# Performance work log

Hardware: AMD Instinct MI355X
Metric: run time of the kernel (lower is better)

Reference implementation:

```python
import jax, jax.numpy as jnp
import numpy as np

N, E, B = 100000, 1600000, 256
IN, H, C = 7, 128, 2
BN_EPS = 1e-5


def setup_inputs() -> dict:
    key = jax.random.key(0)
    ks = jax.random.split(key, 16)
    p = lambda k, s: jax.random.normal(k, s, jnp.float32) * 0.05
    return {
        "x": jax.random.normal(ks[0], (N, IN), jnp.float32),
        "edge_index": jax.random.randint(ks[1], (2, E), 0, N, dtype=jnp.int32),
        "edge_attr": jax.random.normal(ks[2], (E,), jnp.float32),
        "batch": jnp.sort(jax.random.randint(ks[3], (N,), 0, B, dtype=jnp.int32)),
        # GINConv layer 0 MLP: Linear(IN,H) -> ReLU -> Linear(H,H)
        "W0a": p(ks[4], (IN, H)), "b0a": jnp.zeros((H,), jnp.float32),
        "W0b": p(ks[5], (H, H)), "b0b": jnp.zeros((H,), jnp.float32),
        # GINConv layers 1,2 MLPs: Linear(H,H) -> ReLU -> Linear(H,H)
        "W1a": p(ks[6], (H, H)), "b1a": jnp.zeros((H,), jnp.float32),
        "W1b": p(ks[7], (H, H)), "b1b": jnp.zeros((H,), jnp.float32),
        "W2a": p(ks[8], (H, H)), "b2a": jnp.zeros((H,), jnp.float32),
        "W2b": p(ks[9], (H, H)), "b2b": jnp.zeros((H,), jnp.float32),
        # JumpingKnowledge 'cat' projection: Linear(3H, H)
        "Wjk": p(ks[10], (3 * H, H)), "bjk": jnp.zeros((H,), jnp.float32),
        # classifier MLP([H, 2H, C], norm='batch_norm') in eval mode
        "Wc1": p(ks[11], (H, 2 * H)), "bc1": jnp.zeros((2 * H,), jnp.float32),
        "gamma": jnp.ones((2 * H,), jnp.float32),
        "beta": jnp.zeros((2 * H,), jnp.float32),
        "rmean": p(ks[12], (2 * H,)),
        "rvar": jnp.ones((2 * H,), jnp.float32),
        "Wc2": p(ks[13], (2 * H, C)), "bc2": jnp.zeros((C,), jnp.float32),
    }


def _gin_layer(x, src, dst, Wa, ba, Wb, bb):
    # GINConv, eps=0 (train_eps=False): mlp(x_i + sum_{j->i} x_j)
    agg = jax.ops.segment_sum(x[src], dst, num_segments=N)  # [N, d]
    h = x + agg
    h = jax.nn.relu(h @ Wa + ba) @ Wb + bb  # PyG MLP, plain_last, norm=None
    return jax.nn.relu(h)  # BasicGNN inter-layer activation (jk mode: all layers)


def reference(x, edge_index, edge_attr, batch,
              W0a, b0a, W0b, b0b, W1a, b1a, W1b, b1b, W2a, b2a, W2b, b2b,
              Wjk, bjk, Wc1, bc1, gamma, beta, rmean, rvar, Wc2, bc2):
    # NOTE: GINConv does not support edge_weight; PyG BasicGNN drops edge_attr.
    src, dst = edge_index[0], edge_index[1]
    x1 = _gin_layer(x, src, dst, W0a, b0a, W0b, b0b)
    x2 = _gin_layer(x1, src, dst, W1a, b1a, W1b, b1b)
    x3 = _gin_layer(x2, src, dst, W2a, b2a, W2b, b2b)
    h = jnp.concatenate([x1, x2, x3], axis=1) @ Wjk + bjk  # jk='cat' + lin
    pooled = jax.ops.segment_sum(h, batch, num_segments=B)  # global_add_pool [B, H]
    z = pooled @ Wc1 + bc1
    z = (z - rmean) * jax.lax.rsqrt(rvar + BN_EPS) * gamma + beta  # BN eval
    z = jax.nn.relu(z)  # dropout = identity in eval
    return z @ Wc2 + bc2  # [B, C]
```

## Files before the change

kernel.cpp:

```cpp
#include <hip/hip_runtime.h>

#define NN 100000
#define EE 1600000
#define BB 256
#define IN_F 7
#define HH 128
#define NBKT 391
#define BIN_CHUNK 4096
#define BCAP 8192
#define MROWS 16
#define MTHR 128
#define NSB 98

typedef unsigned int uint;
typedef unsigned short ushort;
typedef __attribute__((ext_vector_type(8))) short short8;
typedef __attribute__((ext_vector_type(4))) float f32x4;


__device__ __forceinline__ float bflo(uint u) { return __uint_as_float(u << 16); }
__device__ __forceinline__ float bfhi(uint u) { return __uint_as_float(u & 0xFFFF0000u); }
__device__ __forceinline__ ushort f2bf(float x) {
    uint u = __float_as_uint(x);
    u = (u + 0x7FFFu + ((u >> 16) & 1u)) >> 16;
    return (ushort)u;
}
__device__ __forceinline__ uint packsplit(float v) {
    ushort h = f2bf(v);
    float hf = __uint_as_float((uint)h << 16);
    ushort lo = f2bf(v - hf);
    return ((uint)h << 16) | (uint)lo;
}


__global__ __launch_bounds__(256) void prep(
        const float* __restrict__ w0, const float* __restrict__ w1,
        const float* __restrict__ w2, const float* __restrict__ w3,
        const float* __restrict__ w4, const float* __restrict__ w5,
        const float* __restrict__ w6, const float* __restrict__ w7,
        ushort* __restrict__ hiB, ushort* __restrict__ loB,
        int* __restrict__ deg, int* __restrict__ bcnt,
        float* __restrict__ pooled, int* __restrict__ agg, int n) {
    int b = blockIdx.x, t = threadIdx.x;
    if (b < 512) {
        const float* ws[8] = {w0, w1, w2, w3, w4, w5, w6, w7};
        int gidx = b * 256 + t;
        int mi = gidx >> 14;
        int idx = gidx & 16383;
        int j = idx & 7, l = (idx >> 3) & 63, blk = idx >> 9;
        int kc = blk >> 3, nt = blk & 7;
        int k = kc * 32 + (l >> 4) * 8 + j;
        int nn = nt * 16 + (l & 15);
        float f = ws[mi][k * 128 + nn];
        ushort h = f2bf(f);
        float hf = __uint_as_float((uint)h << 16);
        hiB[gidx] = h;
        loB[gidx] = f2bf(f - hf);
    } else if (b < 512 + NSB) {
        int i = (b - 512) * 1024 + t * 4;
        if (i + 3 < n) {
            *(int4*)&deg[i] = make_int4(0, 0, 0, 0);
        } else {
            #pragma unroll
            for (int k = 0; k < 4; ++k) if (i + k < n) deg[i + k] = 0;
        }
    } else if (b < 512 + NSB + 32) {
        int i = (b - 512 - NSB) * 1024 + t * 4;
        *(float4*)&pooled[i] = make_float4(0.f, 0.f, 0.f, 0.f);
    } else {
        for (int i = t; i < NBKT; i += 256) bcnt[i] = 0;
        if (t < NSB) agg[t] = 0;
    }
}


__global__ __launch_bounds__(256) void bin_count(const int* __restrict__ ei,
        int* __restrict__ deg, int* __restrict__ bcnt, int* __restrict__ ebuf, int e) {
    __shared__ int hist[NBKT];
    __shared__ int base[NBKT];
    int t = threadIdx.x;
    int start = blockIdx.x * BIN_CHUNK;
    int end = start + BIN_CHUNK; if (end > e) end = e;
    for (int b = t; b < NBKT; b += 256) hist[b] = 0;
    __syncthreads();
    for (int i = start + t; i < end; i += 256) {
        int d = ei[e + i];
        atomicAdd(&deg[d], 1);
        atomicAdd(&hist[d >> 8], 1);
    }
    __syncthreads();
    for (int b = t; b < NBKT; b += 256) {
        int c = hist[b];
        base[b] = (c > 0) ? atomicAdd(&bcnt[b], c) : 0;
        hist[b] = 0;
    }
    __syncthreads();
    for (int i = start + t; i < end; i += 256) {
        int d = ei[e + i], s = ei[i];
        int b = d >> 8;
        int pos = base[b] + atomicAdd(&hist[b], 1);
        if (pos < BCAP)
            ebuf[(size_t)b * BCAP + pos] = s | ((d & 255) << 17);
    }
}

__global__ __launch_bounds__(256) void scan_one(const int* __restrict__ deg,
        int* __restrict__ rowptr, int* __restrict__ agg, int n, int e) {
    __shared__ int sd[256];
    __shared__ int red[256];
    int b = blockIdx.x, t = threadIdx.x;
    int base = b * 1024 + t * 4;
    int v[4]; int s = 0;
    #pragma unroll
    for (int k = 0; k < 4; ++k) { int i = base + k; v[k] = (i < n) ? deg[i] : 0; s += v[k]; }
    sd[t] = s; __syncthreads();
    int mine = s;
    for (int off = 1; off < 256; off <<= 1) {
        int add = (t >= off) ? sd[t - off] : 0;
        __syncthreads();
        sd[t] += add;
        __syncthreads();
    }
    if (t == 255) atomicExch(&agg[b], sd[255] + 1);
    int contrib = 0;
    if (t < b) {
        int a;
        do { a = atomicAdd(&agg[t], 0); } while (a == 0);
        contrib = a - 1;
    }
    red[t] = contrib; __syncthreads();
    for (int off = 128; off > 0; off >>= 1) {
        if (t < off) red[t] += red[t + off];
        __syncthreads();
    }
    int run = sd[t] - mine + red[0];
    #pragma unroll
    for (int k = 0; k < 4; ++k) {
        int i = base + k;
        if (i < n) rowptr[i] = run;
        run += v[k];
    }
    if (b == 0 && t == 0) rowptr[n] = e;
}

__global__ __launch_bounds__(256) void distribute(const int* __restrict__ ebuf,
        const int* __restrict__ bcnt, const int* __restrict__ rowptr,
        int* __restrict__ colarr, int n) {
    __shared__ int cur[256];
    int b = blockIdx.x, t = threadIdx.x;
    int n0 = b * 256;
    int n1 = n0 + 256; if (n1 > n) n1 = n;
    if (n0 + t < n1) cur[t] = rowptr[n0 + t];
    __syncthreads();
    int cnt = bcnt[b]; if (cnt > BCAP) cnt = BCAP;
    const int* eb = ebuf + (size_t)b * BCAP;
    for (int i = t; i < cnt; i += 256) {
        int v = eb[i];
        int pos = atomicAdd(&cur[(v >> 17) & 255], 1);
        colarr[pos] = v & 0x1FFFF;
    }
}


__device__ __forceinline__ int swz(int r) { return ((r >> 2) & 7) * 4; }

__device__ __forceinline__ void gemm_mfma(
        const ushort* __restrict__ WH, const ushort* __restrict__ WL,
        const uint (&a_lds)[MROWS][128], int nh, int lm, int lq, int l,
        f32x4 (&acc)[4])
{
    #pragma unroll
    for (int nt = 0; nt < 4; ++nt) acc[nt] = (f32x4){0.f, 0.f, 0.f, 0.f};
    const short8* BH = (const short8*)WH;
    const short8* BL = (const short8*)WL;
    int m = lm;
    int s = swz(m);
    #pragma unroll
    for (int kc = 0; kc < 4; ++kc) {
        int cb = kc * 32 + lq * 8;
        uint4 a0 = *(const uint4*)&a_lds[m][cb ^ s];
        uint4 a1 = *(const uint4*)&a_lds[m][(cb + 4) ^ s];
        uint u[8] = {a0.x, a0.y, a0.z, a0.w, a1.x, a1.y, a1.z, a1.w};
        union { uint d[4]; short8 s8; } ah_, al_;
        #pragma unroll
        for (int p = 0; p < 4; ++p) {
            ah_.d[p] = __builtin_amdgcn_perm(u[2*p+1], u[2*p], 0x07060302u);
            al_.d[p] = __builtin_amdgcn_perm(u[2*p+1], u[2*p], 0x05040100u);
        }
        #pragma unroll
        for (int nt = 0; nt < 4; ++nt) {
            int ntg = nh * 4 + nt;
            short8 bh = BH[(kc * 8 + ntg) * 64 + l];
            short8 bl = BL[(kc * 8 + ntg) * 64 + l];
            acc[nt] = __builtin_amdgcn_mfma_f32_16x16x32_bf16(ah_.s8, bh, acc[nt], 0, 0, 0);
            acc[nt] = __builtin_amdgcn_mfma_f32_16x16x32_bf16(al_.s8, bh, acc[nt], 0, 0, 0);
            acc[nt] = __builtin_amdgcn_mfma_f32_16x16x32_bf16(ah_.s8, bl, acc[nt], 0, 0, 0);
        }
    }
}

__device__ __forceinline__ void epi_store(f32x4 (&acc)[4], const float* __restrict__ bias,
        uint (&a_lds)[MROWS][128], int row0, int n, int nh, int lm, int lq)
{
    #pragma unroll
    for (int nt = 0; nt < 4; ++nt) {
        int col = (nh * 4 + nt) * 16 + lm;
        float bv = bias[col];
        #pragma unroll
        for (int r = 0; r < 4; ++r) {
            int row = lq * 4 + r;
            int gr = row0 + row;
            float v = fmaxf(acc[nt][r] + bv, 0.f);
            if (gr >= n) v = 0.f;
            a_lds[row][col ^ swz(row)] = packsplit(v);
        }
    }
}

template<bool GATHER, bool DO_A, bool LASTB, bool WRITE_X>
__global__ __launch_bounds__(MTHR, 8) void mlp_fused(
        const ushort* __restrict__ in_bf,
        const float* __restrict__ xin,
        const float* __restrict__ W7, const float* __restrict__ b7,
        const int* __restrict__ rowptr, const int* __restrict__ colarr,
        const ushort* __restrict__ WaH, const ushort* __restrict__ WaL,
        const float* __restrict__ ba,
        const ushort* __restrict__ WbH, const ushort* __restrict__ WbL,
        const float* __restrict__ bb,
        const ushort* __restrict__ WjH, const ushort* __restrict__ WjL,
        const float* __restrict__ bjk,
        const int* __restrict__ batch,
        ushort* __restrict__ xout_bf, float* __restrict__ pooled, int n)
{
    __shared__ uint a_lds[MROWS][128];
    __shared__ float h0s[MROWS][8];
    int t = threadIdx.x;
    int row0 = blockIdx.x * MROWS;

    if (GATHER) {
        int* idx_lds = (int*)&a_lds[0][0];
        int rlast = row0 + MROWS; if (rlast > n) rlast = n;
        int eb = rowptr[row0];
        int cnt = rowptr[rlast] - eb;
        int staged = cnt < 2048 ? cnt : 2048;
        for (int i = t; i < staged; i += MTHR)
            idx_lds[i] = __builtin_nontemporal_load(&colarr[eb + i]);
        __syncthreads();

        int r = t >> 3, q = t & 7;
        int gr = row0 + r;
        float f[2][8];
        #pragma unroll
        for (int i = 0; i < 2; ++i)
            #pragma unroll
            for (int j = 0; j < 8; ++j) f[i][j] = 0.f;
        if (gr < n) {
            const uint4* sp = (const uint4*)(in_bf + (size_t)gr * 128);
            #pragma unroll
            for (int i = 0; i < 2; ++i) {
                uint4 v = sp[q + 8 * i];
                f[i][0] = bflo(v.x); f[i][1] = bfhi(v.x);
                f[i][2] = bflo(v.y); f[i][3] = bfhi(v.y);
                f[i][4] = bflo(v.z); f[i][5] = bfhi(v.z);
                f[i][6] = bflo(v.w); f[i][7] = bfhi(v.w);
            }
            int beg = rowptr[gr] - eb, end = rowptr[gr + 1] - eb;
            int j = beg;
            for (; j + 4 <= end; j += 4) {
                int s0 = (j     < staged) ? idx_lds[j]     : colarr[eb + j];
                int s1 = (j + 1 < staged) ? idx_lds[j + 1] : colarr[eb + j + 1];
                int s2 = (j + 2 < staged) ? idx_lds[j + 2] : colarr[eb + j + 2];
                int s3 = (j + 3 < staged) ? idx_lds[j + 3] : colarr[eb + j + 3];
                const uint4* n0 = (const uint4*)(in_bf + (size_t)s0 * 128);
                const uint4* n1 = (const uint4*)(in_bf + (size_t)s1 * 128);
                const uint4* n2 = (const uint4*)(in_bf + (size_t)s2 * 128);
                const uint4* n3 = (const uint4*)(in_bf + (size_t)s3 * 128);
                uint4 v0[2], v1[2], v2[2], v3[2];
                #pragma unroll
                for (int i = 0; i < 2; ++i) {
                    v0[i] = n0[q + 8 * i]; v1[i] = n1[q + 8 * i];
                    v2[i] = n2[q + 8 * i]; v3[i] = n3[q + 8 * i];
                }
                #pragma unroll
                for (int i = 0; i < 2; ++i) {
                    f[i][0] += (bflo(v0[i].x) + bflo(v1[i].x)) + (bflo(v2[i].x) + bflo(v3[i].x));
                    f[i][1] += (bfhi(v0[i].x) + bfhi(v1[i].x)) + (bfhi(v2[i].x) + bfhi(v3[i].x));
                    f[i][2] += (bflo(v0[i].y) + bflo(v1[i].y)) + (bflo(v2[i].y) + bflo(v3[i].y));
                    f[i][3] += (bfhi(v0[i].y) + bfhi(v1[i].y)) + (bfhi(v2[i].y) + bfhi(v3[i].y));
                    f[i][4] += (bflo(v0[i].z) + bflo(v1[i].z)) + (bflo(v2[i].z) + bflo(v3[i].z));
                    f[i][5] += (bfhi(v0[i].z) + bfhi(v1[i].z)) + (bfhi(v2[i].z) + bfhi(v3[i].z));
                    f[i][6] += (bflo(v0[i].w) + bflo(v1[i].w)) + (bflo(v2[i].w) + bflo(v3[i].w));
                    f[i][7] += (bfhi(v0[i].w) + bfhi(v1[i].w)) + (bfhi(v2[i].w) + bfhi(v3[i].w));
                }
            }
            for (; j < end; ++j) {
                int s0 = (j < staged) ? idx_lds[j] : colarr[eb + j];
                const uint4* np = (const uint4*)(in_bf + (size_t)s0 * 128);
                #pragma unroll
                for (int i = 0; i < 2; ++i) {
                    uint4 v = np[q + 8 * i];
                    f[i][0] += bflo(v.x); f[i][1] += bfhi(v.x);
                    f[i][2] += bflo(v.y); f[i][3] += bfhi(v.y);
                    f[i][4] += bflo(v.z); f[i][5] += bfhi(v.z);
                    f[i][6] += bflo(v.w); f[i][7] += bfhi(v.w);
                }
            }
        }
        __syncthreads();
        int s = swz(r);
        #pragma unroll
        for (int i = 0; i < 2; ++i) {
            int c = (q + 8 * i) * 8;
            *(uint4*)&a_lds[r][c ^ s] =
                make_uint4(packsplit(f[i][0]), packsplit(f[i][1]),
                           packsplit(f[i][2]), packsplit(f[i][3]));
            *(uint4*)&a_lds[r][(c + 4) ^ s] =
                make_uint4(packsplit(f[i][4]), packsplit(f[i][5]),
                           packsplit(f[i][6]), packsplit(f[i][7]));
        }
    } else {
        int* idx_lds = (int*)&a_lds[0][0];
        int rlast = row0 + MROWS; if (rlast > n) rlast = n;
        int eb = rowptr[row0];
        int cnt = rowptr[rlast] - eb;
        int staged = cnt < 2048 ? cnt : 2048;
        for (int i = t; i < staged; i += MTHR) idx_lds[i] = colarr[eb + i];
        __syncthreads();

        int r = t >> 3, q = t & 7;
        int gr = row0 + r;
        float aggv = 0.f;
        if (gr < n && q < 7) {
            aggv = xin[gr * 7 + q];
            int beg = rowptr[gr] - eb, end = rowptr[gr + 1] - eb;
            int j = beg;
            for (; j + 2 <= end; j += 2) {
                int s0 = (j     < staged) ? idx_lds[j]     : colarr[eb + j];
                int s1 = (j + 1 < staged) ? idx_lds[j + 1] : colarr[eb + j + 1];
                aggv += xin[s0 * 7 + q] + xin[s1 * 7 + q];
            }
            for (; j < end; ++j) {
                int s0 = (j < staged) ? idx_lds[j] : colarr[eb + j];
                aggv += xin[s0 * 7 + q];
            }
        }
        h0s[r][q] = aggv;
        __syncthreads();

        int c = t;
        float w0r[7];
        #pragma unroll
        for (int k = 0; k < 7; ++k) w0r[k] = W7[k * 128 + c];
        float bv7 = b7[c];
        #pragma unroll
        for (int rr = 0; rr < MROWS; ++rr) {
            float acc7 = bv7;
            #pragma unroll
            for (int k = 0; k < 7; ++k) acc7 += h0s[rr][k] * w0r[k];
            float v = fmaxf(acc7, 0.f);
            if (row0 + rr >= n) v = 0.f;
            a_lds[rr][c ^ swz(rr)] = packsplit(v);
        }
    }
    __syncthreads();

    int w = t >> 6, l = t & 63;
    int nh = w, lm = l & 15, lq = l >> 4;
    f32x4 acc[4];

    if (DO_A) {
        gemm_mfma(WaH, WaL, a_lds, nh, lm, lq, l, acc);
        __syncthreads();
        epi_store(acc, ba, a_lds, row0, n, nh, lm, lq);
        __syncthreads();
    }

    gemm_mfma(WbH, WbL, a_lds, nh, lm, lq, l, acc);
    __syncthreads();
    epi_store(acc, bb, a_lds, row0, n, nh, lm, lq);
    __syncthreads();

    if (WRITE_X) {
        #pragma unroll
        for (int pass = 0; pass < 2; ++pass) {
            int rr = pass * 8 + (t >> 4);
            int gr2 = row0 + rr;
            int c0 = (t & 15) * 8;
            if (gr2 < n) {
                int sw = swz(rr);
                uint p0 = a_lds[rr][(c0 + 0) ^ sw], p1 = a_lds[rr][(c0 + 1) ^ sw];
                uint p2 = a_lds[rr][(c0 + 2) ^ sw], p3 = a_lds[rr][(c0 + 3) ^ sw];
                uint p4 = a_lds[rr][(c0 + 4) ^ sw], p5 = a_lds[rr][(c0 + 5) ^ sw];
                uint p6 = a_lds[rr][(c0 + 6) ^ sw], p7 = a_lds[rr][(c0 + 7) ^ sw];
                uint4 o;
                o.x = __builtin_amdgcn_perm(p1, p0, 0x07060302u);
                o.y = __builtin_amdgcn_perm(p3, p2, 0x07060302u);
                o.z = __builtin_amdgcn_perm(p5, p4, 0x07060302u);
                o.w = __builtin_amdgcn_perm(p7, p6, 0x07060302u);
                *(uint4*)&xout_bf[(size_t)gr2 * 128 + c0] = o;
            }
        }
    }

    gemm_mfma(WjH, WjL, a_lds, nh, lm, lq, l, acc);
    __syncthreads();

    #pragma unroll
    for (int nt = 0; nt < 4; ++nt) {
        int col = (nh * 4 + nt) * 16 + lm;
        float bv = LASTB ? bjk[col] : 0.f;
        #pragma unroll
        for (int r = 0; r < 4; ++r) {
            int row = lq * 4 + r;
            int gr = row0 + row;
            float v = acc[nt][r] + bv;
            if (gr >= n) v = 0.f;
            a_lds[row][col ^ swz(row)] = __float_as_uint(v);
        }
    }
    __syncthreads();

    int row_last = row0 + MROWS - 1; if (row_last > n - 1) row_last = n - 1;
    int g_first = batch[row0];
    int g_last  = batch[row_last];
    int c = t;
    if (g_first == g_last) {
        float sacc = 0.f;
        #pragma unroll
        for (int r = 0; r < MROWS; ++r)
            sacc += __uint_as_float(a_lds[r][c ^ swz(r)]);
        atomicAdd(&pooled[g_first * 128 + c], sacc);
    } else {
        float sacc = 0.f; int gprev = -1;
        for (int r = 0; r < MROWS; ++r) {
            int gr = row0 + r;
            if (gr >= n) break;
            int g = batch[gr];
            if (g != gprev) {
                if (gprev >= 0) atomicAdd(&pooled[gprev * 128 + c], sacc);
                sacc = 0.f; gprev = g;
            }
            sacc += __uint_as_float(a_lds[r][c ^ swz(r)]);
        }
        if (gprev >= 0) atomicAdd(&pooled[gprev * 128 + c], sacc);
    }
}


__global__ __launch_bounds__(256) void classifier(const float* __restrict__ pooled,
        const float* __restrict__ Wc1, const float* __restrict__ bc1,
        const float* __restrict__ gamma, const float* __restrict__ beta,
        const float* __restrict__ rmean, const float* __restrict__ rvar,
        const float* __restrict__ Wc2, const float* __restrict__ bc2,
        float* __restrict__ out) {
    int g = blockIdx.x, t = threadIdx.x;
    __shared__ float p[128];
    __shared__ float r0[256], r1[256];
    if (t < 128) p[t] = pooled[g * 128 + t];
    __syncthreads();
    float acc = bc1[t];
    #pragma unroll 8
    for (int k = 0; k < 128; ++k) acc += p[k] * Wc1[k * 256 + t];
    float z = (acc - rmean[t]) * rsqrtf(rvar[t] + 1e-5f) * gamma[t] + beta[t];
    z = fmaxf(z, 0.f);
    r0[t] = z * Wc2[t * 2 + 0];
    r1[t] = z * Wc2[t * 2 + 1];
    __syncthreads();
    for (int s = 128; s > 0; s >>= 1) {
        if (t < s) { r0[t] += r0[t + s]; r1[t] += r1[t + s]; }
        __syncthreads();
    }
    if (t == 0) {
        out[g * 2 + 0] = r0[0] + bc2[0];
        out[g * 2 + 1] = r1[0] + bc2[1];
    }
}


static inline size_t al256(size_t x) { return (x + 255) & ~size_t(255); }

extern "C" void kernel_launch(void* const* d_in, const int* in_sizes, int n_in,
                              void* d_out, int out_size, void* d_ws, size_t ws_size,
                              hipStream_t stream) {
    const float* x    = (const float*)d_in[0];
    const int*   ei   = (const int*)  d_in[1];
    const int*   batch= (const int*)  d_in[3];
    const float* W0a = (const float*)d_in[4];  const float* b0a = (const float*)d_in[5];
    const float* W0b = (const float*)d_in[6];  const float* b0b = (const float*)d_in[7];
    const float* W1a = (const float*)d_in[8];  const float* b1a = (const float*)d_in[9];
    const float* W1b = (const float*)d_in[10]; const float* b1b = (const float*)d_in[11];
    const float* W2a = (const float*)d_in[12]; const float* b2a = (const float*)d_in[13];
    const float* W2b = (const float*)d_in[14]; const float* b2b = (const float*)d_in[15];
    const float* Wjk = (const float*)d_in[16]; const float* bjk = (const float*)d_in[17];
    const float* Wc1 = (const float*)d_in[18]; const float* bc1 = (const float*)d_in[19];
    const float* gamma=(const float*)d_in[20]; const float* beta= (const float*)d_in[21];
    const float* rmean=(const float*)d_in[22]; const float* rvar= (const float*)d_in[23];
    const float* Wc2 = (const float*)d_in[24]; const float* bc2 = (const float*)d_in[25];
    float* out = (float*)d_out;

    const int N = NN, E = EE, B = BB;

    char* w = (char*)d_ws;
    size_t off = 0;
    int* deg    = (int*)(w + off); off = al256(off + (size_t)N * 4);
    int* rowptr = (int*)(w + off); off = al256(off + (size_t)(N + 1) * 4);
    int* bcnt   = (int*)(w + off); off = al256(off + (size_t)NBKT * 4);
    int* colarr = (int*)(w + off); off = al256(off + (size_t)E * 4);
    int* ebuf   = (int*)(w + off); off = al256(off + (size_t)NBKT * BCAP * 4);
    int* agg    = (int*)(w + off); off = al256(off + 1024 * 4);
    ushort* XB1 = (ushort*)(w + off); off = al256(off + (size_t)N * 128 * 2);
    ushort* XB2 = (ushort*)(w + off); off = al256(off + (size_t)N * 128 * 2);
    float* pooled = (float*)(w + off); off = al256(off + (size_t)B * 128 * 4);
    ushort* wfH = (ushort*)(w + off); off = al256(off + (size_t)8 * 16384 * 2);
    ushort* wfL = (ushort*)(w + off); off = al256(off + (size_t)8 * 16384 * 2);

    prep<<<512 + NSB + 32 + 1, 256, 0, stream>>>(
        W0b, W1a, W1b, W2a, W2b, Wjk, Wjk + 128 * 128, Wjk + 256 * 128,
        wfH, wfL, deg, bcnt, pooled, agg, N);

    bin_count<<<(E + BIN_CHUNK - 1) / BIN_CHUNK, 256, 0, stream>>>(ei, deg, bcnt, ebuf, E);
    scan_one<<<NSB, 256, 0, stream>>>(deg, rowptr, agg, N, E);
    distribute<<<NBKT, 256, 0, stream>>>(ebuf, bcnt, rowptr, colarr, N);

    int gLin = (N + MROWS - 1) / MROWS;

    mlp_fused<false, false, false, true><<<gLin, MTHR, 0, stream>>>(
        nullptr, x, W0a, b0a,
        rowptr, colarr,
        nullptr, nullptr, nullptr,
        wfH + 0 * 16384, wfL + 0 * 16384, b0b,
        wfH + 5 * 16384, wfL + 5 * 16384, nullptr,
        batch, XB1, pooled, N);

    mlp_fused<true, true, false, true><<<gLin, MTHR, 0, stream>>>(
        XB1, nullptr, nullptr, nullptr,
        rowptr, colarr,
        wfH + 1 * 16384, wfL + 1 * 16384, b1a,
        wfH + 2 * 16384, wfL + 2 * 16384, b1b,
        wfH + 6 * 16384, wfL + 6 * 16384, nullptr,
        batch, XB2, pooled, N);

    mlp_fused<true, true, true, false><<<gLin, MTHR, 0, stream>>>(
        XB2, nullptr, nullptr, nullptr,
        rowptr, colarr,
        wfH + 3 * 16384, wfL + 3 * 16384, b2a,
        wfH + 4 * 16384, wfL + 4 * 16384, b2b,
        wfH + 7 * 16384, wfL + 7 * 16384, bjk,
        batch, nullptr, pooled, N);

    classifier<<<B, 256, 0, stream>>>(pooled, Wc1, bc1, gamma, beta,
                                      rmean, rvar, Wc2, bc2, out);
}
```

Before: 358.8 us.

## Derive CSR rowptr from per-bucket counts inside distribute, drop degree atomics and scan

Removes the global per-node degree atomics and the separate decoupled-lookback scan kernel. Each distribute block now sums the preceding bucket counts to get its base offset, stages its bucket's edges in LDS, builds a local per-node histogram and prefix scan, and writes rowptr itself before scattering columns. bin_count also keeps the destination indices in LDS so the second pass does not reload them from global memory. In exchange, every distribute block does a redundant reduction over up to 391 bucket counts and uses about 34KB of LDS, which may reduce occupancy.

```diff
diff --git a/kernel.cpp b/kernel.cpp
--- a/kernel.cpp
+++ b/kernel.cpp
@@ -10,7 +10,6 @@
 #define BCAP 8192
 #define MROWS 16
 #define MTHR 128
-#define NSB 98
 
 typedef unsigned int uint;
 typedef unsigned short ushort;
@@ -39,8 +38,7 @@
         const float* __restrict__ w4, const float* __restrict__ w5,
         const float* __restrict__ w6, const float* __restrict__ w7,
         ushort* __restrict__ hiB, ushort* __restrict__ loB,
-        int* __restrict__ deg, int* __restrict__ bcnt,
-        float* __restrict__ pooled, int* __restrict__ agg, int n) {
+        int* __restrict__ bcnt, float* __restrict__ pooled) {
     int b = blockIdx.x, t = threadIdx.x;
     if (b < 512) {
         const float* ws[8] = {w0, w1, w2, w3, w4, w5, w6, w7};
@@ -56,36 +54,29 @@
         float hf = __uint_as_float((uint)h << 16);
         hiB[gidx] = h;
         loB[gidx] = f2bf(f - hf);
-    } else if (b < 512 + NSB) {
+    } else if (b < 544) {
         int i = (b - 512) * 1024 + t * 4;
-        if (i + 3 < n) {
-            *(int4*)&deg[i] = make_int4(0, 0, 0, 0);
-        } else {
-            #pragma unroll
-            for (int k = 0; k < 4; ++k) if (i + k < n) deg[i + k] = 0;
-        }
-    } else if (b < 512 + NSB + 32) {
-        int i = (b - 512 - NSB) * 1024 + t * 4;
         *(float4*)&pooled[i] = make_float4(0.f, 0.f, 0.f, 0.f);
     } else {
         for (int i = t; i < NBKT; i += 256) bcnt[i] = 0;
-        if (t < NSB) agg[t] = 0;
     }
 }
 
 
 __global__ __launch_bounds__(256) void bin_count(const int* __restrict__ ei,
-        int* __restrict__ deg, int* __restrict__ bcnt, int* __restrict__ ebuf, int e) {
+        int* __restrict__ bcnt, int* __restrict__ ebuf, int e) {
     __shared__ int hist[NBKT];
     __shared__ int base[NBKT];
+    __shared__ int dstb[BIN_CHUNK];
     int t = threadIdx.x;
     int start = blockIdx.x * BIN_CHUNK;
     int end = start + BIN_CHUNK; if (end > e) end = e;
+    int m = end - start;
     for (int b = t; b < NBKT; b += 256) hist[b] = 0;
     __syncthreads();
-    for (int i = start + t; i < end; i += 256) {
-        int d = ei[e + i];
-        atomicAdd(&deg[d], 1);
+    for (int i = t; i < m; i += 256) {
+        int d = ei[e + start + i];
+        dstb[i] = d;
         atomicAdd(&hist[d >> 8], 1);
     }
     __syncthreads();
@@ -95,8 +86,8 @@
         hist[b] = 0;
     }
     __syncthreads();
-    for (int i = start + t; i < end; i += 256) {
-        int d = ei[e + i], s = ei[i];
+    for (int i = t; i < m; i += 256) {
+        int d = dstb[i], s = ei[start + i];
         int b = d >> 8;
         int pos = base[b] + atomicAdd(&hist[b], 1);
         if (pos < BCAP)
@@ -104,58 +95,46 @@
     }
 }
 
-__global__ __launch_bounds__(256) void scan_one(const int* __restrict__ deg,
-        int* __restrict__ rowptr, int* __restrict__ agg, int n, int e) {
-    __shared__ int sd[256];
+__global__ __launch_bounds__(256) void distribute(const int* __restrict__ ebuf,
+        const int* __restrict__ bcnt, int* __restrict__ rowptr,
+        int* __restrict__ colarr, int n, int e) {
+    __shared__ int ent[BCAP];
+    __shared__ int cur[256];
     __shared__ int red[256];
     int b = blockIdx.x, t = threadIdx.x;
-    int base = b * 1024 + t * 4;
-    int v[4]; int s = 0;
-    #pragma unroll
-    for (int k = 0; k < 4; ++k) { int i = base + k; v[k] = (i < n) ? deg[i] : 0; s += v[k]; }
-    sd[t] = s; __syncthreads();
-    int mine = s;
-    for (int off = 1; off < 256; off <<= 1) {
-        int add = (t >= off) ? sd[t - off] : 0;
-        __syncthreads();
-        sd[t] += add;
-        __syncthreads();
-    }
-    if (t == 255) atomicExch(&agg[b], sd[255] + 1);
-    int contrib = 0;
-    if (t < b) {
-        int a;
-        do { a = atomicAdd(&agg[t], 0); } while (a == 0);
-        contrib = a - 1;
-    }
-    red[t] = contrib; __syncthreads();
+    int part = 0;
+    for (int i = t; i < b; i += 256) part += bcnt[i];
+    red[t] = part; __syncthreads();
     for (int off = 128; off > 0; off >>= 1) {
         if (t < off) red[t] += red[t + off];
         __syncthreads();
     }
-    int run = sd[t] - mine + red[0];
-    #pragma unroll
-    for (int k = 0; k < 4; ++k) {
-        int i = base + k;
-        if (i < n) rowptr[i] = run;
-        run += v[k];
-    }
-    if (b == 0 && t == 0) rowptr[n] = e;
-}
-
-__global__ __launch_bounds__(256) void distribute(const int* __restrict__ ebuf,
-        const int* __restrict__ bcnt, const int* __restrict__ rowptr,
-        int* __restrict__ colarr, int n) {
-    __shared__ int cur[256];
-    int b = blockIdx.x, t = threadIdx.x;
-    int n0 = b * 256;
-    int n1 = n0 + 256; if (n1 > n) n1 = n;
-    if (n0 + t < n1) cur[t] = rowptr[n0 + t];
+    int base0 = red[0];
     __syncthreads();
     int cnt = bcnt[b]; if (cnt > BCAP) cnt = BCAP;
     const int* eb = ebuf + (size_t)b * BCAP;
+    for (int i = t; i < cnt; i += 256) ent[i] = eb[i];
+    cur[t] = 0;
+    __syncthreads();
+    for (int i = t; i < cnt; i += 256) atomicAdd(&cur[(ent[i] >> 17) & 255], 1);
+    __syncthreads();
+    int myc = cur[t];
+    red[t] = myc; __syncthreads();
+    for (int off = 1; off < 256; off <<= 1) {
+        int add = (t >= off) ? red[t - off] : 0;
+        __syncthreads();
+        red[t] += add;
+        __syncthreads();
+    }
+    int excl = red[t] - myc;
+    int n0 = b * 256;
+    if (n0 + t < n) rowptr[n0 + t] = base0 + excl;
+    if (b == NBKT - 1 && t == 0) rowptr[n] = e;
+    __syncthreads();
+    cur[t] = base0 + excl;
+    __syncthreads();
     for (int i = t; i < cnt; i += 256) {
-        int v = eb[i];
+        int v = ent[i];
         int pos = atomicAdd(&cur[(v >> 17) & 255], 1);
         colarr[pos] = v & 0x1FFFF;
     }
@@ -502,25 +481,22 @@
 
     char* w = (char*)d_ws;
     size_t off = 0;
-    int* deg    = (int*)(w + off); off = al256(off + (size_t)N * 4);
     int* rowptr = (int*)(w + off); off = al256(off + (size_t)(N + 1) * 4);
     int* bcnt   = (int*)(w + off); off = al256(off + (size_t)NBKT * 4);
     int* colarr = (int*)(w + off); off = al256(off + (size_t)E * 4);
     int* ebuf   = (int*)(w + off); off = al256(off + (size_t)NBKT * BCAP * 4);
-    int* agg    = (int*)(w + off); off = al256(off + 1024 * 4);
     ushort* XB1 = (ushort*)(w + off); off = al256(off + (size_t)N * 128 * 2);
     ushort* XB2 = (ushort*)(w + off); off = al256(off + (size_t)N * 128 * 2);
     float* pooled = (float*)(w + off); off = al256(off + (size_t)B * 128 * 4);
     ushort* wfH = (ushort*)(w + off); off = al256(off + (size_t)8 * 16384 * 2);
     ushort* wfL = (ushort*)(w + off); off = al256(off + (size_t)8 * 16384 * 2);
 
-    prep<<<512 + NSB + 32 + 1, 256, 0, stream>>>(
+    prep<<<545, 256, 0, stream>>>(
         W0b, W1a, W1b, W2a, W2b, Wjk, Wjk + 128 * 128, Wjk + 256 * 128,
-        wfH, wfL, deg, bcnt, pooled, agg, N);
-
-    bin_count<<<(E + BIN_CHUNK - 1) / BIN_CHUNK, 256, 0, stream>>>(ei, deg, bcnt, ebuf, E);
-    scan_one<<<NSB, 256, 0, stream>>>(deg, rowptr, agg, N, E);
-    distribute<<<NBKT, 256, 0, stream>>>(ebuf, bcnt, rowptr, colarr, N);
+        wfH, wfL, bcnt, pooled);
+
+    bin_count<<<(E + BIN_CHUNK - 1) / BIN_CHUNK, 256, 0, stream>>>(ei, bcnt, ebuf, E);
+    distribute<<<NBKT, 256, 0, stream>>>(ebuf, bcnt, rowptr, colarr, N, E);
 
     int gLin = (N + MROWS - 1) / MROWS;
 
```

New measurement: 297.7 us (median of 2 runs). 17.0% less time.
